# Optimization experiments

Measured on AMD Instinct MI355X. Metric: run time of the kernel, lower is better.

The kernel has to match this reference:

```python
import jax, jax.numpy as jnp
import numpy as np

B, H, L, K = 4096, 2048, 16384, 32

def setup_inputs() -> dict:
    key = jax.random.key(0)
    k1, k2, k3 = jax.random.split(key, 3)
    x = jax.random.normal(k1, (B, H), dtype=jnp.float32)
    W_enc = jax.random.normal(k2, (L, H), dtype=jnp.float32) * (1.0 / np.sqrt(H))
    W_dec = jax.random.normal(k3, (H, L), dtype=jnp.float32)
    # normalize_decoder(): unit norm along dim=0 (hidden axis), per latent column
    W_dec = W_dec / jnp.linalg.norm(W_dec, axis=0, keepdims=True)
    return {"x": x, "W_enc": W_enc, "W_dec": W_dec, "topk": K}

def reference(x, W_enc, W_dec, topk):
    # encoder: z = relu(x @ W_enc^T)   [B, L]
    z_pre = jnp.einsum('bh,lh->bl', x, W_enc)
    z_relu = jax.nn.relu(z_pre)
    # top-k along last dim, scatter values into zeros (sparse latent code)
    vals, idx = jax.lax.top_k(z_relu, topk)            # [B, K]
    rows = jnp.arange(z_relu.shape[0])[:, None]        # [B, 1]
    z = jnp.zeros_like(z_relu).at[rows, idx].set(vals)  # [B, L]
    # decoder: x_hat = z @ W_dec^T    [B, H]
    x_hat = jnp.einsum('bl,hl->bh', z, W_dec)
    return (x_hat, z)
```

## Files before the change

### kernel.cpp

```cpp
#include <hip/hip_runtime.h>

#define B_ROWS 4096
#define H_DIM  2048
#define L_DIM  16384
#define TOPK   32
#define CAND_CAP 512
#define AMBIG_CAP 128
#define BAND 0.06f

typedef __attribute__((ext_vector_type(8))) short bf16x8;
typedef __attribute__((ext_vector_type(4))) float f32x4;

__device__ __forceinline__ unsigned short f32_to_bf16(float f) {
  unsigned int u = __float_as_uint(f);
  u += 0x7FFFu + ((u >> 16) & 1u);
  return (unsigned short)(u >> 16);
}
__device__ __forceinline__ float bf16_to_f32(unsigned short h) {
  return __uint_as_float(((unsigned int)h) << 16);
}

__device__ __forceinline__ void gload_lds16(const void* g, void* l) {
  __builtin_amdgcn_global_load_lds(
      (const __attribute__((address_space(1))) unsigned int*)g,
      (__attribute__((address_space(3))) unsigned int*)l, 16, 0, 0);
}

__global__ __launch_bounds__(256) void k_convert(const float* __restrict__ src,
                                                 unsigned short* __restrict__ dst, int n4) {
  int i = blockIdx.x * 256 + threadIdx.x;
  if (i < n4) {
    float4 v = ((const float4*)src)[i];
    ushort4 o;
    o.x = f32_to_bf16(v.x); o.y = f32_to_bf16(v.y);
    o.z = f32_to_bf16(v.z); o.w = f32_to_bf16(v.w);
    ((ushort4*)dst)[i] = o;
  }
}

__global__ __launch_bounds__(256) void k_transpose(const float* __restrict__ Wd,
                                                   unsigned short* __restrict__ WdT) {
  __shared__ float tile[64][65];
  int bi = blockIdx.x & 255;
  int bj = blockIdx.x >> 8;
  int t = threadIdx.x;
  int l0 = bi * 64, h0 = bj * 64;
#pragma unroll
  for (int p = 0; p < 4; ++p) {
    int hr = p * 16 + (t >> 4);
    int lc = (t & 15) * 4;
    float4 v = *(const float4*)(Wd + (size_t)(h0 + hr) * L_DIM + l0 + lc);
    tile[lc + 0][hr] = v.x; tile[lc + 1][hr] = v.y;
    tile[lc + 2][hr] = v.z; tile[lc + 3][hr] = v.w;
  }
  __syncthreads();
#pragma unroll
  for (int p = 0; p < 2; ++p) {
    int lr = p * 32 + (t >> 3);
    int hc = (t & 7) * 8;
    bf16x8 o;
#pragma unroll
    for (int i = 0; i < 8; ++i) o[i] = (short)f32_to_bf16(tile[lr][hc + i]);
    *(bf16x8*)(WdT + (size_t)(l0 + lr) * H_DIM + h0 + hc) = o;
  }
}

__global__ __launch_bounds__(512, 2) void k_gemm(const unsigned short* __restrict__ A,
                                                 const unsigned short* __restrict__ Bm,
                                                 unsigned short* __restrict__ Zp) {
  __shared__ unsigned short As[3 * 8192];
  __shared__ unsigned short Bs[3 * 8192];
  const size_t K = H_DIM;
  int bid = blockIdx.x;
  int cpx = gridDim.x >> 3;
  int swz = (bid & 7) * cpx + (bid >> 3);
  int tm = swz >> 6;
  int tn = swz & 63;
  int t = threadIdx.x;
  int lane = t & 63;
  int w = t >> 6;
  int wm = w >> 2, wn = w & 3;

  int rloc = lane & 15;
  int kc = lane >> 4;
  int swzk = (kc ^ ((rloc >> 1) & 3)) << 3;

  int srow = t >> 2;
  int kcs = (t & 3) ^ ((srow >> 1) & 3);
  const unsigned short* aS0 = A + (size_t)(tm * 256 + srow) * K + kcs * 8;
  const unsigned short* aS1 = aS0 + 128 * K;
  const unsigned short* bS0 = Bm + (size_t)(tn * 256 + srow) * K + kcs * 8;
  const unsigned short* bS1 = bS0 + 128 * K;
  int dA = t * 8;

  f32x4 acc[8][4];
#pragma unroll
  for (int i = 0; i < 8; ++i)
#pragma unroll
    for (int j = 0; j < 4; ++j) { f32x4 z = {0.f, 0.f, 0.f, 0.f}; acc[i][j] = z; }

#define STAGE_A(kt, sw) { size_t ko = (size_t)(kt) * 32; \
    gload_lds16(aS0 + ko, &As[(sw) * 8192 + dA]); \
    gload_lds16(aS1 + ko, &As[(sw) * 8192 + 4096 + dA]); }
#define STAGE_B(kt, sw) { size_t ko = (size_t)(kt) * 32; \
    gload_lds16(bS0 + ko, &Bs[(sw) * 8192 + dA]); \
    gload_lds16(bS1 + ko, &Bs[(sw) * 8192 + 4096 + dA]); }

  STAGE_A(0, 0) STAGE_B(0, 0)
  STAGE_A(1, 1) STAGE_B(1, 1)
  asm volatile("s_waitcnt vmcnt(4)" ::: "memory");
  __builtin_amdgcn_s_barrier();

  int sR = 0;
  const int aBase0 = (wm * 128 + rloc) * 32 + swzk;
  const int bBase0 = (wn * 64 + rloc) * 32 + swzk;
  const int NKT = H_DIM / 32;
  for (int kt = 0; kt < NKT; ++kt) {
    int sW = sR + 2; if (sW >= 3) sW -= 3;
    const unsigned short* Ab = &As[sR * 8192 + aBase0];
    const unsigned short* Bb = &Bs[sR * 8192 + bBase0];
    bool st = (kt + 2 < NKT);
    bf16x8 a0[4], b0[4];
#pragma unroll
    for (int m = 0; m < 4; ++m) a0[m] = *(const bf16x8*)(Ab + m * 512);
#pragma unroll
    for (int n = 0; n < 4; ++n) b0[n] = *(const bf16x8*)(Bb + n * 512);
    if (st) STAGE_A(kt + 2, sW)
    __builtin_amdgcn_s_barrier();
    __builtin_amdgcn_s_setprio(1);
#pragma unroll
    for (int m = 0; m < 4; ++m)
#pragma unroll
      for (int n = 0; n < 4; ++n)
        acc[m][n] = __builtin_amdgcn_mfma_f32_16x16x32_bf16(a0[m], b0[n], acc[m][n], 0, 0, 0);
    __builtin_amdgcn_s_setprio(0);
    __builtin_amdgcn_s_barrier();
    bf16x8 a1[4];
#pragma unroll
    for (int m = 0; m < 4; ++m) a1[m] = *(const bf16x8*)(Ab + (m + 4) * 512);
    if (st) STAGE_B(kt + 2, sW)
    __builtin_amdgcn_s_barrier();
    __builtin_amdgcn_s_setprio(1);
#pragma unroll
    for (int m = 0; m < 4; ++m)
#pragma unroll
      for (int n = 0; n < 4; ++n)
        acc[m + 4][n] = __builtin_amdgcn_mfma_f32_16x16x32_bf16(a1[m], b0[n], acc[m + 4][n], 0, 0, 0);
    __builtin_amdgcn_s_setprio(0);
    if (kt < NKT - 2) { asm volatile("s_waitcnt vmcnt(4)" ::: "memory"); }
    else if (kt == NKT - 2) { asm volatile("s_waitcnt vmcnt(0)" ::: "memory"); }
    __builtin_amdgcn_s_barrier();
    ++sR; if (sR == 3) sR = 0;
  }
#undef STAGE_A
#undef STAGE_B
  int colg = lane & 15, quad = lane >> 4;
  size_t rbase = (size_t)(tm * 256 + wm * 128 + quad * 4);
  int cbase = tn * 256 + wn * 64 + colg;
#pragma unroll
  for (int m = 0; m < 8; ++m)
#pragma unroll
    for (int n = 0; n < 4; ++n) {
      size_t rr = rbase + m * 16;
      int cc = cbase + n * 16;
#pragma unroll
      for (int r = 0; r < 4; ++r)
        Zp[(rr + r) * L_DIM + cc] = f32_to_bf16(fmaxf(acc[m][n][r], 0.0f));
    }
}

__global__ __launch_bounds__(256) void k_collect(const unsigned short* __restrict__ zp,
                                                 int* __restrict__ cidx,
                                                 float* __restrict__ cvals,
                                                 int* __restrict__ ccnt) {
  int b = blockIdx.x;
  const bf16x8* row = (const bf16x8*)(zp + (size_t)b * L_DIM);
  __shared__ unsigned int s_cnt;
  int t = threadIdx.x;
  float thr = 2.3f;
  for (int attempt = 0; attempt < 8; ++attempt) {
    if (t == 0) s_cnt = 0;
    __syncthreads();
    for (int i = t; i < L_DIM / 8; i += 256) {
      bf16x8 v = row[i];
#pragma unroll
      for (int q = 0; q < 8; ++q) {
        float f = bf16_to_f32((unsigned short)v[q]);
        if (f > thr) {
          unsigned int p = atomicAdd(&s_cnt, 1u);
          if (p < CAND_CAP) { cidx[b * CAND_CAP + p] = i * 8 + q; cvals[b * CAND_CAP + p] = f; }
        }
      }
    }
    __syncthreads();
    if (s_cnt >= 40 || thr <= 0.0f) break;
    thr -= 0.6f; if (thr < 0.0f) thr = 0.0f;
    __syncthreads();
  }
  if (t == 0) ccnt[b] = (int)(s_cnt < CAND_CAP ? s_cnt : CAND_CAP);
}

__global__ __launch_bounds__(256) void k_topk(const float* __restrict__ x,
                                              const float* __restrict__ Wenc,
                                              const int* __restrict__ cidx,
                                              const float* __restrict__ cvals,
                                              const int* __restrict__ ccnt,
                                              float* __restrict__ zout,
                                              float* __restrict__ selv,
                                              int* __restrict__ seli) {
  int b = blockIdx.x;
  int t = threadIdx.x;
  __shared__ float xr[H_DIM];
  __shared__ float cv[CAND_CAP];
  __shared__ int   ci[CAND_CAP];
  __shared__ float s_b32;
  __shared__ unsigned int s_na, s_nin;
  __shared__ int    ai[AMBIG_CAP];
  __shared__ double ax[AMBIG_CAP];
  int cnt = ccnt[b]; if (cnt > CAND_CAP) cnt = CAND_CAP;

  const float4* xv = (const float4*)(x + (size_t)b * H_DIM);
  for (int i = t; i < H_DIM / 4; i += 256) ((float4*)xr)[i] = xv[i];
  for (int i = t; i < cnt; i += 256) { cv[i] = cvals[b * CAND_CAP + i]; ci[i] = cidx[b * CAND_CAP + i]; }
  if (t == 0) { s_b32 = -1.0f; s_na = 0; s_nin = 0; }
  {
    float4 zz = {0.f, 0.f, 0.f, 0.f};
    float4* zrow = (float4*)(zout + (size_t)b * L_DIM);
#pragma unroll
    for (int i = 0; i < L_DIM / 4 / 256; ++i) zrow[i * 256 + t] = zz;
  }
  __syncthreads();

  bool tiny = (cnt < TOPK);

  if (!tiny) {
    for (int i = t; i < cnt; i += 256) {
      float vi = cv[i]; int r = 0;
      for (int j = 0; j < cnt; ++j) { float vj = cv[j]; r += (vj > vi) || (vj == vi && j < i); }
      if (r == 31) s_b32 = vi;
    }
  }
  __syncthreads();
  float b32 = s_b32;

  if (!tiny) {
    for (int i = t; i < cnt; i += 256) {
      if (fabsf(cv[i] - b32) <= BAND) {
        unsigned int p = atomicAdd(&s_na, 1u);
        if (p < AMBIG_CAP) ai[p] = i;
      }
    }
  }
  __syncthreads();
  int na = (int)(s_na < AMBIG_CAP ? s_na : AMBIG_CAP);

  int wv = t >> 6, lane = t & 63;
  for (int a = wv; a < na; a += 4) {
    int l = ci[ai[a]];
    const float4* wrow = (const float4*)(Wenc + (size_t)l * H_DIM);
    double acc = 0.0;
#pragma unroll
    for (int k8 = 0; k8 < 8; ++k8) {
      float4 ww = wrow[k8 * 64 + lane];
      float4 xx = ((const float4*)xr)[k8 * 64 + lane];
      acc += (double)ww.x * xx.x + (double)ww.y * xx.y + (double)ww.z * xx.z + (double)ww.w * xx.w;
    }
#pragma unroll
    for (int s = 32; s; s >>= 1) acc += __shfl_xor(acc, s, 64);
    if (lane == 0) ax[a] = acc;
  }
  __syncthreads();

  for (int i = t; i < cnt; i += 256) {
    float vi = cv[i];
    if (tiny || vi - b32 > BAND) {
      unsigned int p = atomicAdd(&s_nin, 1u);
      selv[b * TOPK + p] = vi; seli[b * TOPK + p] = ci[i];
      zout[(size_t)b * L_DIM + ci[i]] = vi;
    }
  }
  __syncthreads();
  int s0 = (int)s_nin;

  if (t < 64) {
    int need = TOPK - s0; if (need < 0) need = 0;
    for (int k = 0; k < need; ++k) {
      double bv = -1.0e300; int bidx = 0x7fffffff; int bpos = -1;
      for (int a = lane; a < na; a += 64) {
        double v = ax[a]; int ii = ci[ai[a]];
        if (v > bv || (v == bv && ii < bidx)) { bv = v; bidx = ii; bpos = a; }
      }
#pragma unroll
      for (int sh = 32; sh; sh >>= 1) {
        double ov = __shfl_xor(bv, sh, 64);
        int oi = __shfl_xor(bidx, sh, 64);
        int op = __shfl_xor(bpos, sh, 64);
        if (ov > bv || (ov == bv && oi < bidx)) { bv = ov; bidx = oi; bpos = op; }
      }
      bool valid = (bpos >= 0) && (bv > -1.0e299);
      if (lane == 0) {
        selv[b * TOPK + s0 + k] = valid ? (float)bv : 0.0f;
        seli[b * TOPK + s0 + k] = valid ? bidx : 0;
        if (valid) zout[(size_t)b * L_DIM + bidx] = (float)bv;
      }
      for (int a = lane; a < na; a += 64) if (a == bpos) ax[a] = -1.0e300;
    }
  }
}

__global__ __launch_bounds__(256) void k_decoder(const unsigned short* __restrict__ WdT,
                                                 const float* __restrict__ selv,
                                                 const int* __restrict__ seli,
                                                 float* __restrict__ xhat) {
  int b = blockIdx.x;
  int t = threadIdx.x;
  __shared__ float sv[TOPK];
  __shared__ int si[TOPK];
  if (t < TOPK) { sv[t] = selv[b * TOPK + t]; si[t] = seli[b * TOPK + t]; }
  __syncthreads();
  float acc[8] = {0.f, 0.f, 0.f, 0.f, 0.f, 0.f, 0.f, 0.f};
  for (int j = 0; j < TOPK; ++j) {
    float vj = sv[j];
    bf16x8 w = *(const bf16x8*)(WdT + (size_t)si[j] * H_DIM + t * 8);
#pragma unroll
    for (int i = 0; i < 8; ++i) acc[i] += vj * bf16_to_f32((unsigned short)w[i]);
  }
  float4 o0 = {acc[0], acc[1], acc[2], acc[3]};
  float4 o1 = {acc[4], acc[5], acc[6], acc[7]};
  float4* op = (float4*)(xhat + (size_t)b * H_DIM + t * 8);
  op[0] = o0; op[1] = o1;
}

extern "C" void kernel_launch(void* const* d_in, const int* in_sizes, int n_in,
                              void* d_out, int out_size, void* d_ws, size_t ws_size,
                              hipStream_t stream) {
  const float* x    = (const float*)d_in[0];
  const float* Wenc = (const float*)d_in[1];
  const float* Wdec = (const float*)d_in[2];

  float* xhat = (float*)d_out;
  float* z    = (float*)d_out + (size_t)B_ROWS * H_DIM;

  char* ws = (char*)d_ws;
  if (ws_size < 168837120u) return;
  unsigned short* xbf    = (unsigned short*)(ws);
  unsigned short* Wencbf = (unsigned short*)(ws + 16777216);
  unsigned short* WdT    = (unsigned short*)(ws + 83886080);
  int*    cidx  = (int*)  (ws + 150994944);
  float*  cvals = (float*)(ws + 159383552);
  int*    ccnt  = (int*)  (ws + 167772160);
  float*  selv  = (float*)(ws + 167788544);
  int*    seli  = (int*)  (ws + 168312832);

  unsigned short* zpre = (unsigned short*)z;

  k_convert<<<(2097152 + 255) / 256, 256, 0, stream>>>(x, xbf, 2097152);
  k_convert<<<(8388608 + 255) / 256, 256, 0, stream>>>(Wenc, Wencbf, 8388608);
  k_transpose<<<8192, 256, 0, stream>>>(Wdec, WdT);
  k_gemm<<<1024, 512, 0, stream>>>(xbf, Wencbf, zpre);
  k_collect<<<B_ROWS, 256, 0, stream>>>(zpre, cidx, cvals, ccnt);
  k_topk<<<B_ROWS, 256, 0, stream>>>(x, Wenc, cidx, cvals, ccnt, z, selv, seli);
  k_decoder<<<B_ROWS, 256, 0, stream>>>(WdT, selv, seli, xhat);
}
```

Before: 662.3 us.

## Fuse collect, top-k and decoder into one per-row kernel with in-place bf16 scratch

Merges the candidate collection, exact top-k refinement and sparse decoder into a single per-row kernel that keeps candidates and the selected set in shared memory instead of global workspace. The bf16 pre-activation is now written with a doubled row stride, so each row's bf16 data sits in the first half of that row's own fp32 output slot and can be read and then overwritten by the zero fill in the same block. This removes two kernel launches and the global round trips for candidates and selections. The cost is higher shared memory per block, which may lower occupancy, and a correctness dependence on the read-before-overwrite ordering within each row.

```diff
diff --git a/kernel.cpp b/kernel.cpp
--- a/kernel.cpp
+++ b/kernel.cpp
@@ -7,6 +7,7 @@
 #define CAND_CAP 512
 #define AMBIG_CAP 128
 #define BAND 0.06f
+#define ZP_STRIDE (2 * L_DIM)
 
 typedef __attribute__((ext_vector_type(8))) short bf16x8;
 typedef __attribute__((ext_vector_type(4))) float f32x4;
@@ -165,18 +166,31 @@
       int cc = cbase + n * 16;
 #pragma unroll
       for (int r = 0; r < 4; ++r)
-        Zp[(rr + r) * L_DIM + cc] = f32_to_bf16(fmaxf(acc[m][n][r], 0.0f));
-    }
-}
-
-__global__ __launch_bounds__(256) void k_collect(const unsigned short* __restrict__ zp,
-                                                 int* __restrict__ cidx,
-                                                 float* __restrict__ cvals,
-                                                 int* __restrict__ ccnt) {
+        Zp[(rr + r) * ZP_STRIDE + cc] = f32_to_bf16(fmaxf(acc[m][n][r], 0.0f));
+    }
+}
+
+__global__ __launch_bounds__(256) void k_finish(const float* __restrict__ x,
+                                                const float* __restrict__ Wenc,
+                                                const unsigned short* __restrict__ WdT,
+                                                float* __restrict__ zout,
+                                                float* __restrict__ xhat) {
   int b = blockIdx.x;
-  const bf16x8* row = (const bf16x8*)(zp + (size_t)b * L_DIM);
-  __shared__ unsigned int s_cnt;
   int t = threadIdx.x;
+  __shared__ float xr[H_DIM];
+  __shared__ float cv[CAND_CAP];
+  __shared__ int   ci[CAND_CAP];
+  __shared__ float s_b32;
+  __shared__ unsigned int s_cnt, s_na, s_nin;
+  __shared__ int    ai[AMBIG_CAP];
+  __shared__ double ax[AMBIG_CAP];
+  __shared__ float  sv[TOPK];
+  __shared__ int    si[TOPK];
+
+  const bf16x8* row = (const bf16x8*)((const unsigned short*)zout + (size_t)b * ZP_STRIDE);
+  const float4* xv = (const float4*)(x + (size_t)b * H_DIM);
+  for (int i = t; i < H_DIM / 4; i += 256) ((float4*)xr)[i] = xv[i];
+
   float thr = 2.3f;
   for (int attempt = 0; attempt < 8; ++attempt) {
     if (t == 0) s_cnt = 0;
@@ -188,7 +202,7 @@
         float f = bf16_to_f32((unsigned short)v[q]);
         if (f > thr) {
           unsigned int p = atomicAdd(&s_cnt, 1u);
-          if (p < CAND_CAP) { cidx[b * CAND_CAP + p] = i * 8 + q; cvals[b * CAND_CAP + p] = f; }
+          if (p < CAND_CAP) { ci[p] = i * 8 + q; cv[p] = f; }
         }
       }
     }
@@ -197,38 +211,16 @@
     thr -= 0.6f; if (thr < 0.0f) thr = 0.0f;
     __syncthreads();
   }
-  if (t == 0) ccnt[b] = (int)(s_cnt < CAND_CAP ? s_cnt : CAND_CAP);
-}
-
-__global__ __launch_bounds__(256) void k_topk(const float* __restrict__ x,
-                                              const float* __restrict__ Wenc,
-                                              const int* __restrict__ cidx,
-                                              const float* __restrict__ cvals,
-                                              const int* __restrict__ ccnt,
-                                              float* __restrict__ zout,
-                                              float* __restrict__ selv,
-                                              int* __restrict__ seli) {
-  int b = blockIdx.x;
-  int t = threadIdx.x;
-  __shared__ float xr[H_DIM];
-  __shared__ float cv[CAND_CAP];
-  __shared__ int   ci[CAND_CAP];
-  __shared__ float s_b32;
-  __shared__ unsigned int s_na, s_nin;
-  __shared__ int    ai[AMBIG_CAP];
-  __shared__ double ax[AMBIG_CAP];
-  int cnt = ccnt[b]; if (cnt > CAND_CAP) cnt = CAND_CAP;
-
-  const float4* xv = (const float4*)(x + (size_t)b * H_DIM);
-  for (int i = t; i < H_DIM / 4; i += 256) ((float4*)xr)[i] = xv[i];
-  for (int i = t; i < cnt; i += 256) { cv[i] = cvals[b * CAND_CAP + i]; ci[i] = cidx[b * CAND_CAP + i]; }
-  if (t == 0) { s_b32 = -1.0f; s_na = 0; s_nin = 0; }
+  int cnt = (int)(s_cnt < CAND_CAP ? s_cnt : CAND_CAP);
+
+  __syncthreads();
   {
     float4 zz = {0.f, 0.f, 0.f, 0.f};
-    float4* zrow = (float4*)(zout + (size_t)b * L_DIM);
-#pragma unroll
-    for (int i = 0; i < L_DIM / 4 / 256; ++i) zrow[i * 256 + t] = zz;
-  }
+    float4* zr = (float4*)(zout + (size_t)b * L_DIM);
+#pragma unroll
+    for (int i = 0; i < L_DIM / 4 / 256; ++i) zr[i * 256 + t] = zz;
+  }
+  if (t == 0) { s_b32 = -1.0f; s_na = 0; s_nin = 0; }
   __syncthreads();
 
   bool tiny = (cnt < TOPK);
@@ -275,7 +267,7 @@
     float vi = cv[i];
     if (tiny || vi - b32 > BAND) {
       unsigned int p = atomicAdd(&s_nin, 1u);
-      selv[b * TOPK + p] = vi; seli[b * TOPK + p] = ci[i];
+      sv[p] = vi; si[p] = ci[i];
       zout[(size_t)b * L_DIM + ci[i]] = vi;
     }
   }
@@ -299,31 +291,21 @@
       }
       bool valid = (bpos >= 0) && (bv > -1.0e299);
       if (lane == 0) {
-        selv[b * TOPK + s0 + k] = valid ? (float)bv : 0.0f;
-        seli[b * TOPK + s0 + k] = valid ? bidx : 0;
+        sv[s0 + k] = valid ? (float)bv : 0.0f;
+        si[s0 + k] = valid ? bidx : 0;
         if (valid) zout[(size_t)b * L_DIM + bidx] = (float)bv;
       }
       for (int a = lane; a < na; a += 64) if (a == bpos) ax[a] = -1.0e300;
     }
   }
-}
-
-__global__ __launch_bounds__(256) void k_decoder(const unsigned short* __restrict__ WdT,
-                                                 const float* __restrict__ selv,
-                                                 const int* __restrict__ seli,
-                                                 float* __restrict__ xhat) {
-  int b = blockIdx.x;
-  int t = threadIdx.x;
-  __shared__ float sv[TOPK];
-  __shared__ int si[TOPK];
-  if (t < TOPK) { sv[t] = selv[b * TOPK + t]; si[t] = seli[b * TOPK + t]; }
-  __syncthreads();
+  __syncthreads();
+
   float acc[8] = {0.f, 0.f, 0.f, 0.f, 0.f, 0.f, 0.f, 0.f};
   for (int j = 0; j < TOPK; ++j) {
     float vj = sv[j];
-    bf16x8 w = *(const bf16x8*)(WdT + (size_t)si[j] * H_DIM + t * 8);
-#pragma unroll
-    for (int i = 0; i < 8; ++i) acc[i] += vj * bf16_to_f32((unsigned short)w[i]);
+    bf16x8 ww = *(const bf16x8*)(WdT + (size_t)si[j] * H_DIM + t * 8);
+#pragma unroll
+    for (int i = 0; i < 8; ++i) acc[i] += vj * bf16_to_f32((unsigned short)ww[i]);
   }
   float4 o0 = {acc[0], acc[1], acc[2], acc[3]};
   float4 o1 = {acc[4], acc[5], acc[6], acc[7]};
@@ -342,15 +324,10 @@
   float* z    = (float*)d_out + (size_t)B_ROWS * H_DIM;
 
   char* ws = (char*)d_ws;
-  if (ws_size < 168837120u) return;
+  if (ws_size < 150994944u) return;
   unsigned short* xbf    = (unsigned short*)(ws);
   unsigned short* Wencbf = (unsigned short*)(ws + 16777216);
   unsigned short* WdT    = (unsigned short*)(ws + 83886080);
-  int*    cidx  = (int*)  (ws + 150994944);
-  float*  cvals = (float*)(ws + 159383552);
-  int*    ccnt  = (int*)  (ws + 167772160);
-  float*  selv  = (float*)(ws + 167788544);
-  int*    seli  = (int*)  (ws + 168312832);
 
   unsigned short* zpre = (unsigned short*)z;
 
@@ -358,7 +335,5 @@
   k_convert<<<(8388608 + 255) / 256, 256, 0, stream>>>(Wenc, Wencbf, 8388608);
   k_transpose<<<8192, 256, 0, stream>>>(Wdec, WdT);
   k_gemm<<<1024, 512, 0, stream>>>(xbf, Wencbf, zpre);
-  k_collect<<<B_ROWS, 256, 0, stream>>>(zpre, cidx, cvals, ccnt);
-  k_topk<<<B_ROWS, 256, 0, stream>>>(x, Wenc, cidx, cvals, ccnt, z, selv, seli);
-  k_decoder<<<B_ROWS, 256, 0, stream>>>(WdT, selv, seli, xhat);
-}
+  k_finish<<<B_ROWS, 256, 0, stream>>>(x, Wenc, WdT, z, xhat);
+}
```

Measured after the change: 641.0 us. 3.2% less time.
